# Kernel optimization log

Hardware: AMD Instinct MI355X
Metric: run time of the kernel (lower is better)

Reference implementation:

```python
import jax, jax.numpy as jnp
import numpy as np

N = 50000   # nodes
E = 640000  # edges
IN = 128
HID = 128
EPS = 1e-5


def setup_inputs() -> dict:
    key = jax.random.key(0)
    ks = jax.random.split(key, 8)
    s = 1.0 / np.sqrt(IN)
    inp = {
        "x": jax.random.normal(ks[0], (N, IN), jnp.float32),
        "src": jax.random.randint(ks[1], (E,), 0, N, dtype=jnp.int32),
        "dst": jax.random.randint(ks[2], (E,), 0, N, dtype=jnp.int32),
        "W1": jax.random.normal(ks[3], (IN, HID), jnp.float32) * s,
        "b1": jnp.zeros((HID,), jnp.float32),
        "g1": jnp.ones((HID,), jnp.float32),
        "be1": jnp.zeros((HID,), jnp.float32),
        "W2": jax.random.normal(ks[4], (HID, HID), jnp.float32) * s,
        "b2": jnp.zeros((HID,), jnp.float32),
        "g2": jnp.ones((HID,), jnp.float32),
        "be2": jnp.zeros((HID,), jnp.float32),
        "W3": jax.random.normal(ks[5], (HID, HID), jnp.float32) * s,
        "b3": jnp.zeros((HID,), jnp.float32),
        "g3": jnp.ones((HID,), jnp.float32),
        "be3": jnp.zeros((HID,), jnp.float32),
    }
    return inp


def _layernorm(h, g, b):
    mu = jnp.mean(h, axis=-1, keepdims=True)
    var = jnp.mean(jnp.square(h - mu), axis=-1, keepdims=True)
    return g * (h - mu) * jax.lax.rsqrt(var + EPS) + b


def _gcn_conv(h, W, b, src, dst):
    # Kipf & Welling GCN: D^{-1/2} (A + I) D^{-1/2} (H W) + b
    # self-loops added with weight 1; degree computed on the target index.
    hw = h @ W                                          # [N, HID]
    deg = jax.ops.segment_sum(jnp.ones((E,), h.dtype), dst, num_segments=N) + 1.0
    dinv = jax.lax.rsqrt(deg)                           # deg >= 1 due to self loop
    msg = hw[src] * (dinv[src] * dinv[dst])[:, None]    # gather + normalize, [E, HID]
    agg = jax.ops.segment_sum(msg, dst, num_segments=N)  # scatter-add
    agg = agg + hw * (dinv * dinv)[:, None]             # self-loop contribution
    return agg + b


def reference(x, src, dst, W1, b1, g1, be1, W2, b2, g2, be2, W3, b3, g3, be3):
    layers = [(W1, b1, g1, be1), (W2, b2, g2, be2), (W3, b3, g3, be3)]
    h = x
    for i, (W, b, g, be) in enumerate(layers):
        h_in = h
        h = _gcn_conv(h, W, b, src, dst)
        h = _layernorm(h, g, be)
        h = jax.nn.relu(h)
        # dropout: eval mode -> identity
        if i > 0 and h.shape == h_in.shape:
            h = h + h_in
    return h
```

## Files before the change

kernel.cpp:

```cpp
#include <hip/hip_runtime.h>
#include <hip/hip_bf16.h>

#define NFEAT 128
#define EPSLN 1e-5f
#define PAD 64

typedef __attribute__((ext_vector_type(8))) short short8;
typedef __attribute__((ext_vector_type(4))) float f32x4;

__device__ __forceinline__ float bf2f(ushort u) {
    union { uint u32; float f; } v; v.u32 = ((uint)u) << 16; return v.f;
}
__device__ __forceinline__ ushort f2bf(float f) {
    union { float f; uint u32; } v; v.f = f;
    uint u = v.u32;
    u += 0x7FFF + ((u >> 16) & 1);
    return (ushort)(u >> 16);
}

__global__ void setup_kernel(const float* __restrict__ x, ushort* __restrict__ xb, int n4,
                             int4* __restrict__ cnt4, int ncnt4,
                             const float* __restrict__ W0, const float* __restrict__ W1,
                             const float* __restrict__ W2,
                             ushort* __restrict__ Wt0, ushort* __restrict__ Wt1,
                             ushort* __restrict__ Wt2) {
    int i = blockIdx.x * 256 + threadIdx.x;
    if (i < n4) {
        float4 v = ((const float4*)x)[i];
        ushort4 o;
        o.x = f2bf(v.x); o.y = f2bf(v.y); o.z = f2bf(v.z); o.w = f2bf(v.w);
        ((ushort4*)xb)[i] = o;
    }
    if (i < ncnt4) cnt4[i] = make_int4(0, 0, 0, 0);
    if (i < 3 * NFEAT * NFEAT) {
        int l = i / (NFEAT * NFEAT);
        int r = i - l * (NFEAT * NFEAT);
        int k = r >> 7, n = r & 127;
        const float* W = (l == 0) ? W0 : (l == 1) ? W1 : W2;
        ushort* Wt = (l == 0) ? Wt0 : (l == 1) ? Wt1 : Wt2;
        Wt[n * NFEAT + k] = f2bf(W[r]);
    }
}

__global__ void fill_kernel(const int* __restrict__ src, const int* __restrict__ dst,
                            int* __restrict__ cnt, int* __restrict__ csr, int E) {
    int e = blockIdx.x * 256 + threadIdx.x;
    if (e < E) {
        int d = dst[e];
        int s = src[e];
        int pos = atomicAdd(&cnt[d], 1);
        if (pos < PAD) csr[d * PAD + pos] = s;
    }
}

__global__ __launch_bounds__(256) void gemm_mfma_kernel(const ushort* __restrict__ hb,
                                                        const ushort* __restrict__ Wt,
                                                        const int* __restrict__ cnt,
                                                        ushort* __restrict__ hw, int N) {
    __shared__ ushort WtL[NFEAT * NFEAT];
    {
        const uint4* src4 = (const uint4*)Wt;
        uint4* dst4 = (uint4*)WtL;
        #pragma unroll
        for (int i = 0; i < 8; ++i)
            dst4[threadIdx.x + i * 256] = src4[threadIdx.x + i * 256];
    }
    __syncthreads();

    const int wave = threadIdx.x >> 6;
    const int lane = threadIdx.x & 63;
    const int quad = lane >> 4;
    const int l16  = lane & 15;
    const int row0 = blockIdx.x * 128 + wave * 32;

    short8 afrag[2][4];
    #pragma unroll
    for (int t = 0; t < 2; ++t) {
        const int arow = row0 + t * 16 + l16;
        const short8* ap = (const short8*)(hb + (size_t)arow * NFEAT);
        const bool rowok = (arow < N);
        #pragma unroll
        for (int ks = 0; ks < 4; ++ks) {
            if (rowok) afrag[t][ks] = ap[ks * 4 + quad];
            else       afrag[t][ks] = short8{0, 0, 0, 0, 0, 0, 0, 0};
        }
    }

    f32x4 acc[2][8];
    #pragma unroll
    for (int t = 0; t < 2; ++t)
        #pragma unroll
        for (int ct = 0; ct < 8; ++ct) acc[t][ct] = f32x4{0.f, 0.f, 0.f, 0.f};

    #pragma unroll
    for (int ct = 0; ct < 8; ++ct) {
        const int bcol = ct * 16 + l16;
        const short8* bp = (const short8*)(WtL + (size_t)bcol * NFEAT);
        #pragma unroll
        for (int ks = 0; ks < 4; ++ks) {
            short8 bfrag = bp[ks * 4 + quad];
            acc[0][ct] = __builtin_amdgcn_mfma_f32_16x16x32_bf16(afrag[0][ks], bfrag, acc[0][ct], 0, 0, 0);
            acc[1][ct] = __builtin_amdgcn_mfma_f32_16x16x32_bf16(afrag[1][ks], bfrag, acc[1][ct], 0, 0, 0);
        }
    }

    #pragma unroll
    for (int t = 0; t < 2; ++t) {
        const int orow_base = row0 + t * 16 + quad * 4;
        #pragma unroll
        for (int r = 0; r < 4; ++r) {
            const int orow = orow_base + r;
            if (orow < N) {
                const float di = rsqrtf((float)cnt[orow] + 1.0f);
                ushort* op = hw + (size_t)orow * NFEAT + l16;
                #pragma unroll
                for (int ct = 0; ct < 8; ++ct)
                    op[ct * 16] = f2bf(acc[t][ct][r] * di);
            }
        }
    }
}

__global__ __launch_bounds__(256) void agg_ln_kernel(const ushort* __restrict__ hwb,
                                                     const int* __restrict__ cnt,
                                                     const int* __restrict__ csr,
                                                     const float* __restrict__ bias,
                                                     const float* __restrict__ gamma,
                                                     const float* __restrict__ beta,
                                                     const ushort* __restrict__ hres_b,
                                                     float* __restrict__ outf,
                                                     ushort* __restrict__ outb,
                                                     int N) {
    const int node = blockIdx.x * 4 + (threadIdx.x >> 6);
    const int lane = threadIdx.x & 63;
    if (node >= N) return;
    const int quad = lane >> 4;
    const int l16  = lane & 15;

    const int cn  = cnt[node];
    const int deg = (cn < PAD) ? cn : PAD;
    const float di = rsqrtf((float)cn + 1.0f);
    const int* ce = csr + (size_t)node * PAD;
    const uint4* hw4 = (const uint4*)hwb;

    float acc[8];
    #pragma unroll
    for (int i = 0; i < 8; ++i) acc[i] = 0.f;

    const int ng = (deg + 7) >> 3;
    for (int gi = 0; gi < ng; ++gi) {
        const int j0 = gi * 8 + quad;
        const int j1 = j0 + 4;
        int s0 = 0, s1 = 0;
        float w0 = 0.f, w1 = 0.f;
        if (j0 < deg) { s0 = ce[j0]; w0 = 1.f; }
        if (j1 < deg) { s1 = ce[j1]; w1 = 1.f; }
        uint4 v0 = hw4[(size_t)s0 * 16 + l16];
        uint4 v1 = hw4[(size_t)s1 * 16 + l16];
        acc[0] = fmaf(bf2f((ushort)(v0.x & 0xFFFF)), w0, acc[0]);
        acc[1] = fmaf(bf2f((ushort)(v0.x >> 16)),   w0, acc[1]);
        acc[2] = fmaf(bf2f((ushort)(v0.y & 0xFFFF)), w0, acc[2]);
        acc[3] = fmaf(bf2f((ushort)(v0.y >> 16)),   w0, acc[3]);
        acc[4] = fmaf(bf2f((ushort)(v0.z & 0xFFFF)), w0, acc[4]);
        acc[5] = fmaf(bf2f((ushort)(v0.z >> 16)),   w0, acc[5]);
        acc[6] = fmaf(bf2f((ushort)(v0.w & 0xFFFF)), w0, acc[6]);
        acc[7] = fmaf(bf2f((ushort)(v0.w >> 16)),   w0, acc[7]);
        acc[0] = fmaf(bf2f((ushort)(v1.x & 0xFFFF)), w1, acc[0]);
        acc[1] = fmaf(bf2f((ushort)(v1.x >> 16)),   w1, acc[1]);
        acc[2] = fmaf(bf2f((ushort)(v1.y & 0xFFFF)), w1, acc[2]);
        acc[3] = fmaf(bf2f((ushort)(v1.y >> 16)),   w1, acc[3]);
        acc[4] = fmaf(bf2f((ushort)(v1.z & 0xFFFF)), w1, acc[4]);
        acc[5] = fmaf(bf2f((ushort)(v1.z >> 16)),   w1, acc[5]);
        acc[6] = fmaf(bf2f((ushort)(v1.w & 0xFFFF)), w1, acc[6]);
        acc[7] = fmaf(bf2f((ushort)(v1.w >> 16)),   w1, acc[7]);
    }

    #pragma unroll
    for (int i = 0; i < 8; ++i) {
        acc[i] += __shfl_xor(acc[i], 16);
        acc[i] += __shfl_xor(acc[i], 32);
    }

    const int c0i = l16 * 8;
    uint4 hv = hw4[(size_t)node * 16 + l16];
    float4 b0 = ((const float4*)(bias + c0i))[0];
    float4 b1 = ((const float4*)(bias + c0i))[1];
    float x[8];
    x[0] = (acc[0] + bf2f((ushort)(hv.x & 0xFFFF))) * di + b0.x;
    x[1] = (acc[1] + bf2f((ushort)(hv.x >> 16)))   * di + b0.y;
    x[2] = (acc[2] + bf2f((ushort)(hv.y & 0xFFFF))) * di + b0.z;
    x[3] = (acc[3] + bf2f((ushort)(hv.y >> 16)))   * di + b0.w;
    x[4] = (acc[4] + bf2f((ushort)(hv.z & 0xFFFF))) * di + b1.x;
    x[5] = (acc[5] + bf2f((ushort)(hv.z >> 16)))   * di + b1.y;
    x[6] = (acc[6] + bf2f((ushort)(hv.w & 0xFFFF))) * di + b1.z;
    x[7] = (acc[7] + bf2f((ushort)(hv.w >> 16)))   * di + b1.w;

    float s = 0.f, sq = 0.f;
    #pragma unroll
    for (int i = 0; i < 8; ++i) { s += x[i]; sq += x[i] * x[i]; }
    #pragma unroll
    for (int o = 8; o > 0; o >>= 1) {
        s  += __shfl_xor(s, o);
        sq += __shfl_xor(sq, o);
    }
    const float mu  = s * (1.0f / NFEAT);
    const float var = sq * (1.0f / NFEAT) - mu * mu;
    const float rs  = rsqrtf(var + EPSLN);

    float4 g0 = ((const float4*)(gamma + c0i))[0];
    float4 g1 = ((const float4*)(gamma + c0i))[1];
    float4 e0 = ((const float4*)(beta + c0i))[0];
    float4 e1 = ((const float4*)(beta + c0i))[1];
    float gm[8] = {g0.x, g0.y, g0.z, g0.w, g1.x, g1.y, g1.z, g1.w};
    float bt[8] = {e0.x, e0.y, e0.z, e0.w, e1.x, e1.y, e1.z, e1.w};

    float y[8];
    #pragma unroll
    for (int i = 0; i < 8; ++i)
        y[i] = fmaxf(gm[i] * (x[i] - mu) * rs + bt[i], 0.0f);

    if (hres_b) {
        uint4 hr = ((const uint4*)hres_b)[(size_t)node * 16 + l16];
        y[0] += bf2f((ushort)(hr.x & 0xFFFF));
        y[1] += bf2f((ushort)(hr.x >> 16));
        y[2] += bf2f((ushort)(hr.y & 0xFFFF));
        y[3] += bf2f((ushort)(hr.y >> 16));
        y[4] += bf2f((ushort)(hr.z & 0xFFFF));
        y[5] += bf2f((ushort)(hr.z >> 16));
        y[6] += bf2f((ushort)(hr.w & 0xFFFF));
        y[7] += bf2f((ushort)(hr.w >> 16));
    }

    if (quad == 0) {
        if (outf) {
            float4* op = (float4*)(outf + (size_t)node * NFEAT + c0i);
            op[0] = make_float4(y[0], y[1], y[2], y[3]);
            op[1] = make_float4(y[4], y[5], y[6], y[7]);
        }
        if (outb) {
            uint4 ob;
            ob.x = (uint)f2bf(y[0]) | ((uint)f2bf(y[1]) << 16);
            ob.y = (uint)f2bf(y[2]) | ((uint)f2bf(y[3]) << 16);
            ob.z = (uint)f2bf(y[4]) | ((uint)f2bf(y[5]) << 16);
            ob.w = (uint)f2bf(y[6]) | ((uint)f2bf(y[7]) << 16);
            ((uint4*)outb)[(size_t)node * 16 + l16] = ob;
        }
    }
}

extern "C" void kernel_launch(void* const* d_in, const int* in_sizes, int n_in,
                              void* d_out, int out_size, void* d_ws, size_t ws_size,
                              hipStream_t stream) {
    const float* x   = (const float*)d_in[0];
    const int*   src = (const int*)d_in[1];
    const int*   dst = (const int*)d_in[2];
    const float* W[3]  = {(const float*)d_in[3], (const float*)d_in[7],  (const float*)d_in[11]};
    const float* b[3]  = {(const float*)d_in[4], (const float*)d_in[8],  (const float*)d_in[12]};
    const float* g[3]  = {(const float*)d_in[5], (const float*)d_in[9],  (const float*)d_in[13]};
    const float* be[3] = {(const float*)d_in[6], (const float*)d_in[10], (const float*)d_in[14]};

    const int N = in_sizes[0] / NFEAT;
    const int E = in_sizes[1];

    char* ws = (char*)d_ws;
    size_t off = 0;
    auto carve = [&](size_t bytes) -> char* {
        char* p = ws + off;
        off = (off + bytes + 255) & ~(size_t)255;
        return p;
    };
    const int ncnt4 = (N + 3) / 4;
    int*    cnt = (int*)   carve((size_t)ncnt4 * 4 * sizeof(int));
    int*    csr = (int*)   carve(((size_t)N * PAD + 64) * sizeof(int));
    ushort* hwb = (ushort*)carve((size_t)N * NFEAT * sizeof(ushort));
    ushort* xb  = (ushort*)carve((size_t)N * NFEAT * sizeof(ushort));
    ushort* h1b = (ushort*)carve((size_t)N * NFEAT * sizeof(ushort));
    ushort* h2b = (ushort*)carve((size_t)N * NFEAT * sizeof(ushort));
    ushort* Wt[3];
    for (int l = 0; l < 3; ++l) Wt[l] = (ushort*)carve(NFEAT * NFEAT * sizeof(ushort));
    (void)ws_size;

    const int n4 = N * NFEAT / 4;
    int setup_threads = n4;
    if (3 * NFEAT * NFEAT > setup_threads) setup_threads = 3 * NFEAT * NFEAT;
    if (ncnt4 > setup_threads) setup_threads = ncnt4;
    setup_kernel<<<(setup_threads + 255) / 256, 256, 0, stream>>>(
        x, xb, n4, (int4*)cnt, ncnt4, W[0], W[1], W[2], Wt[0], Wt[1], Wt[2]);

    fill_kernel<<<(E + 255) / 256, 256, 0, stream>>>(src, dst, cnt, csr, E);

    const ushort* hbin[3]  = {xb, h1b, h2b};
    const ushort* hresb[3] = {nullptr, h1b, h2b};
    float*        houtf[3] = {nullptr, nullptr, (float*)d_out};
    ushort*       houtb[3] = {h1b, h2b, nullptr};

    const int gemm_blocks = (N + 127) / 128;
    const int agg_blocks = (N + 3) / 4;

    for (int l = 0; l < 3; ++l) {
        gemm_mfma_kernel<<<gemm_blocks, 256, 0, stream>>>(hbin[l], Wt[l], cnt, hwb, N);
        agg_ln_kernel<<<agg_blocks, 256, 0, stream>>>(hwb, cnt, csr,
                                                      b[l], g[l], be[l],
                                                      hresb[l], houtf[l], houtb[l], N);
    }
}
```

Before: 282.7 us.

## Fuse x bf16 conversion into first GEMM, shrink GEMM tile, deepen gather unroll

The standalone fp32-to-bf16 conversion of x is removed from the setup kernel. The first-layer GEMM now reads fp32 x directly and converts it in registers, which drops a full write and re-read of the intermediate bf16 buffer. The GEMM tile shrinks from 128 to 64 rows per block (16 rows per wave), giving twice as many blocks but less reuse of the LDS-resident weights. The aggregation kernel issues four neighbor gathers per iteration instead of two and hoists the self, bias, gamma, beta and residual loads ahead of the gather loop to add memory-level parallelism, at the cost of more registers.

```diff
diff --git a/kernel.cpp b/kernel.cpp
--- a/kernel.cpp
+++ b/kernel.cpp
@@ -18,19 +18,12 @@
     return (ushort)(u >> 16);
 }
 
-__global__ void setup_kernel(const float* __restrict__ x, ushort* __restrict__ xb, int n4,
-                             int4* __restrict__ cnt4, int ncnt4,
+__global__ void setup_kernel(int4* __restrict__ cnt4, int ncnt4,
                              const float* __restrict__ W0, const float* __restrict__ W1,
                              const float* __restrict__ W2,
                              ushort* __restrict__ Wt0, ushort* __restrict__ Wt1,
                              ushort* __restrict__ Wt2) {
     int i = blockIdx.x * 256 + threadIdx.x;
-    if (i < n4) {
-        float4 v = ((const float4*)x)[i];
-        ushort4 o;
-        o.x = f2bf(v.x); o.y = f2bf(v.y); o.z = f2bf(v.z); o.w = f2bf(v.w);
-        ((ushort4*)xb)[i] = o;
-    }
     if (i < ncnt4) cnt4[i] = make_int4(0, 0, 0, 0);
     if (i < 3 * NFEAT * NFEAT) {
         int l = i / (NFEAT * NFEAT);
@@ -54,6 +47,7 @@
 }
 
 __global__ __launch_bounds__(256) void gemm_mfma_kernel(const ushort* __restrict__ hb,
+                                                        const float* __restrict__ hf,
                                                         const ushort* __restrict__ Wt,
                                                         const int* __restrict__ cnt,
                                                         ushort* __restrict__ hw, int N) {
@@ -71,26 +65,38 @@
     const int lane = threadIdx.x & 63;
     const int quad = lane >> 4;
     const int l16  = lane & 15;
-    const int row0 = blockIdx.x * 128 + wave * 32;
-
-    short8 afrag[2][4];
-    #pragma unroll
-    for (int t = 0; t < 2; ++t) {
-        const int arow = row0 + t * 16 + l16;
+    const int row0 = blockIdx.x * 64 + wave * 16;
+    const int arow = row0 + l16;
+    const bool rowok = (arow < N);
+
+    short8 afrag[4];
+    if (hf) {
+        const float4* fp = (const float4*)(hf + (size_t)arow * NFEAT);
+        #pragma unroll
+        for (int ks = 0; ks < 4; ++ks) {
+            short8 a = short8{0, 0, 0, 0, 0, 0, 0, 0};
+            if (rowok) {
+                float4 u0 = fp[ks * 8 + quad * 2];
+                float4 u1 = fp[ks * 8 + quad * 2 + 1];
+                a[0] = (short)f2bf(u0.x); a[1] = (short)f2bf(u0.y);
+                a[2] = (short)f2bf(u0.z); a[3] = (short)f2bf(u0.w);
+                a[4] = (short)f2bf(u1.x); a[5] = (short)f2bf(u1.y);
+                a[6] = (short)f2bf(u1.z); a[7] = (short)f2bf(u1.w);
+            }
+            afrag[ks] = a;
+        }
+    } else {
         const short8* ap = (const short8*)(hb + (size_t)arow * NFEAT);
-        const bool rowok = (arow < N);
         #pragma unroll
         for (int ks = 0; ks < 4; ++ks) {
-            if (rowok) afrag[t][ks] = ap[ks * 4 + quad];
-            else       afrag[t][ks] = short8{0, 0, 0, 0, 0, 0, 0, 0};
-        }
-    }
-
-    f32x4 acc[2][8];
-    #pragma unroll
-    for (int t = 0; t < 2; ++t)
-        #pragma unroll
-        for (int ct = 0; ct < 8; ++ct) acc[t][ct] = f32x4{0.f, 0.f, 0.f, 0.f};
+            if (rowok) afrag[ks] = ap[ks * 4 + quad];
+            else       afrag[ks] = short8{0, 0, 0, 0, 0, 0, 0, 0};
+        }
+    }
+
+    f32x4 acc[8];
+    #pragma unroll
+    for (int ct = 0; ct < 8; ++ct) acc[ct] = f32x4{0.f, 0.f, 0.f, 0.f};
 
     #pragma unroll
     for (int ct = 0; ct < 8; ++ct) {
@@ -99,24 +105,20 @@
         #pragma unroll
         for (int ks = 0; ks < 4; ++ks) {
             short8 bfrag = bp[ks * 4 + quad];
-            acc[0][ct] = __builtin_amdgcn_mfma_f32_16x16x32_bf16(afrag[0][ks], bfrag, acc[0][ct], 0, 0, 0);
-            acc[1][ct] = __builtin_amdgcn_mfma_f32_16x16x32_bf16(afrag[1][ks], bfrag, acc[1][ct], 0, 0, 0);
-        }
-    }
-
-    #pragma unroll
-    for (int t = 0; t < 2; ++t) {
-        const int orow_base = row0 + t * 16 + quad * 4;
-        #pragma unroll
-        for (int r = 0; r < 4; ++r) {
-            const int orow = orow_base + r;
-            if (orow < N) {
-                const float di = rsqrtf((float)cnt[orow] + 1.0f);
-                ushort* op = hw + (size_t)orow * NFEAT + l16;
-                #pragma unroll
-                for (int ct = 0; ct < 8; ++ct)
-                    op[ct * 16] = f2bf(acc[t][ct][r] * di);
-            }
+            acc[ct] = __builtin_amdgcn_mfma_f32_16x16x32_bf16(afrag[ks], bfrag, acc[ct], 0, 0, 0);
+        }
+    }
+
+    const int orow_base = row0 + quad * 4;
+    #pragma unroll
+    for (int r = 0; r < 4; ++r) {
+        const int orow = orow_base + r;
+        if (orow < N) {
+            const float di = rsqrtf((float)cnt[orow] + 1.0f);
+            ushort* op = hw + (size_t)orow * NFEAT + l16;
+            #pragma unroll
+            for (int ct = 0; ct < 8; ++ct)
+                op[ct * 16] = f2bf(acc[ct][r] * di);
         }
     }
 }
@@ -136,6 +138,7 @@
     if (node >= N) return;
     const int quad = lane >> 4;
     const int l16  = lane & 15;
+    const int c0i  = l16 * 8;
 
     const int cn  = cnt[node];
     const int deg = (cn < PAD) ? cn : PAD;
@@ -143,36 +146,67 @@
     const int* ce = csr + (size_t)node * PAD;
     const uint4* hw4 = (const uint4*)hwb;
 
+    uint4 hv = hw4[(size_t)node * 16 + l16];
+    float4 b0 = ((const float4*)(bias + c0i))[0];
+    float4 b1 = ((const float4*)(bias + c0i))[1];
+    float4 g0 = ((const float4*)(gamma + c0i))[0];
+    float4 g1 = ((const float4*)(gamma + c0i))[1];
+    float4 e0 = ((const float4*)(beta + c0i))[0];
+    float4 e1 = ((const float4*)(beta + c0i))[1];
+    uint4 hr = make_uint4(0, 0, 0, 0);
+    if (hres_b) hr = ((const uint4*)hres_b)[(size_t)node * 16 + l16];
+
     float acc[8];
     #pragma unroll
     for (int i = 0; i < 8; ++i) acc[i] = 0.f;
 
-    const int ng = (deg + 7) >> 3;
+    const int ng = (deg + 15) >> 4;
     for (int gi = 0; gi < ng; ++gi) {
-        const int j0 = gi * 8 + quad;
-        const int j1 = j0 + 4;
-        int s0 = 0, s1 = 0;
-        float w0 = 0.f, w1 = 0.f;
-        if (j0 < deg) { s0 = ce[j0]; w0 = 1.f; }
-        if (j1 < deg) { s1 = ce[j1]; w1 = 1.f; }
-        uint4 v0 = hw4[(size_t)s0 * 16 + l16];
-        uint4 v1 = hw4[(size_t)s1 * 16 + l16];
-        acc[0] = fmaf(bf2f((ushort)(v0.x & 0xFFFF)), w0, acc[0]);
-        acc[1] = fmaf(bf2f((ushort)(v0.x >> 16)),   w0, acc[1]);
-        acc[2] = fmaf(bf2f((ushort)(v0.y & 0xFFFF)), w0, acc[2]);
-        acc[3] = fmaf(bf2f((ushort)(v0.y >> 16)),   w0, acc[3]);
-        acc[4] = fmaf(bf2f((ushort)(v0.z & 0xFFFF)), w0, acc[4]);
-        acc[5] = fmaf(bf2f((ushort)(v0.z >> 16)),   w0, acc[5]);
-        acc[6] = fmaf(bf2f((ushort)(v0.w & 0xFFFF)), w0, acc[6]);
-        acc[7] = fmaf(bf2f((ushort)(v0.w >> 16)),   w0, acc[7]);
-        acc[0] = fmaf(bf2f((ushort)(v1.x & 0xFFFF)), w1, acc[0]);
-        acc[1] = fmaf(bf2f((ushort)(v1.x >> 16)),   w1, acc[1]);
-        acc[2] = fmaf(bf2f((ushort)(v1.y & 0xFFFF)), w1, acc[2]);
-        acc[3] = fmaf(bf2f((ushort)(v1.y >> 16)),   w1, acc[3]);
-        acc[4] = fmaf(bf2f((ushort)(v1.z & 0xFFFF)), w1, acc[4]);
-        acc[5] = fmaf(bf2f((ushort)(v1.z >> 16)),   w1, acc[5]);
-        acc[6] = fmaf(bf2f((ushort)(v1.w & 0xFFFF)), w1, acc[6]);
-        acc[7] = fmaf(bf2f((ushort)(v1.w >> 16)),   w1, acc[7]);
+        const int jb = gi * 16 + quad;
+        int   s[4];
+        float w[4];
+        #pragma unroll
+        for (int u = 0; u < 4; ++u) {
+            const int j = jb + u * 4;
+            if (j < deg) { s[u] = ce[j]; w[u] = 1.f; }
+            else         { s[u] = 0;     w[u] = 0.f; }
+        }
+        uint4 v0 = hw4[(size_t)s[0] * 16 + l16];
+        uint4 v1 = hw4[(size_t)s[1] * 16 + l16];
+        uint4 v2 = hw4[(size_t)s[2] * 16 + l16];
+        uint4 v3 = hw4[(size_t)s[3] * 16 + l16];
+        acc[0] = fmaf(bf2f((ushort)(v0.x & 0xFFFF)), w[0], acc[0]);
+        acc[1] = fmaf(bf2f((ushort)(v0.x >> 16)),   w[0], acc[1]);
+        acc[2] = fmaf(bf2f((ushort)(v0.y & 0xFFFF)), w[0], acc[2]);
+        acc[3] = fmaf(bf2f((ushort)(v0.y >> 16)),   w[0], acc[3]);
+        acc[4] = fmaf(bf2f((ushort)(v0.z & 0xFFFF)), w[0], acc[4]);
+        acc[5] = fmaf(bf2f((ushort)(v0.z >> 16)),   w[0], acc[5]);
+        acc[6] = fmaf(bf2f((ushort)(v0.w & 0xFFFF)), w[0], acc[6]);
+        acc[7] = fmaf(bf2f((ushort)(v0.w >> 16)),   w[0], acc[7]);
+        acc[0] = fmaf(bf2f((ushort)(v1.x & 0xFFFF)), w[1], acc[0]);
+        acc[1] = fmaf(bf2f((ushort)(v1.x >> 16)),   w[1], acc[1]);
+        acc[2] = fmaf(bf2f((ushort)(v1.y & 0xFFFF)), w[1], acc[2]);
+        acc[3] = fmaf(bf2f((ushort)(v1.y >> 16)),   w[1], acc[3]);
+        acc[4] = fmaf(bf2f((ushort)(v1.z & 0xFFFF)), w[1], acc[4]);
+        acc[5] = fmaf(bf2f((ushort)(v1.z >> 16)),   w[1], acc[5]);
+        acc[6] = fmaf(bf2f((ushort)(v1.w & 0xFFFF)), w[1], acc[6]);
+        acc[7] = fmaf(bf2f((ushort)(v1.w >> 16)),   w[1], acc[7]);
+        acc[0] = fmaf(bf2f((ushort)(v2.x & 0xFFFF)), w[2], acc[0]);
+        acc[1] = fmaf(bf2f((ushort)(v2.x >> 16)),   w[2], acc[1]);
+        acc[2] = fmaf(bf2f((ushort)(v2.y & 0xFFFF)), w[2], acc[2]);
+        acc[3] = fmaf(bf2f((ushort)(v2.y >> 16)),   w[2], acc[3]);
+        acc[4] = fmaf(bf2f((ushort)(v2.z & 0xFFFF)), w[2], acc[4]);
+        acc[5] = fmaf(bf2f((ushort)(v2.z >> 16)),   w[2], acc[5]);
+        acc[6] = fmaf(bf2f((ushort)(v2.w & 0xFFFF)), w[2], acc[6]);
+        acc[7] = fmaf(bf2f((ushort)(v2.w >> 16)),   w[2], acc[7]);
+        acc[0] = fmaf(bf2f((ushort)(v3.x & 0xFFFF)), w[3], acc[0]);
+        acc[1] = fmaf(bf2f((ushort)(v3.x >> 16)),   w[3], acc[1]);
+        acc[2] = fmaf(bf2f((ushort)(v3.y & 0xFFFF)), w[3], acc[2]);
+        acc[3] = fmaf(bf2f((ushort)(v3.y >> 16)),   w[3], acc[3]);
+        acc[4] = fmaf(bf2f((ushort)(v3.z & 0xFFFF)), w[3], acc[4]);
+        acc[5] = fmaf(bf2f((ushort)(v3.z >> 16)),   w[3], acc[5]);
+        acc[6] = fmaf(bf2f((ushort)(v3.w & 0xFFFF)), w[3], acc[6]);
+        acc[7] = fmaf(bf2f((ushort)(v3.w >> 16)),   w[3], acc[7]);
     }
 
     #pragma unroll
@@ -181,10 +215,6 @@
         acc[i] += __shfl_xor(acc[i], 32);
     }
 
-    const int c0i = l16 * 8;
-    uint4 hv = hw4[(size_t)node * 16 + l16];
-    float4 b0 = ((const float4*)(bias + c0i))[0];
-    float4 b1 = ((const float4*)(bias + c0i))[1];
     float x[8];
     x[0] = (acc[0] + bf2f((ushort)(hv.x & 0xFFFF))) * di + b0.x;
     x[1] = (acc[1] + bf2f((ushort)(hv.x >> 16)))   * di + b0.y;
@@ -207,10 +237,6 @@
     const float var = sq * (1.0f / NFEAT) - mu * mu;
     const float rs  = rsqrtf(var + EPSLN);
 
-    float4 g0 = ((const float4*)(gamma + c0i))[0];
-    float4 g1 = ((const float4*)(gamma + c0i))[1];
-    float4 e0 = ((const float4*)(beta + c0i))[0];
-    float4 e1 = ((const float4*)(beta + c0i))[1];
     float gm[8] = {g0.x, g0.y, g0.z, g0.w, g1.x, g1.y, g1.z, g1.w};
     float bt[8] = {e0.x, e0.y, e0.z, e0.w, e1.x, e1.y, e1.z, e1.w};
 
@@ -220,7 +246,6 @@
         y[i] = fmaxf(gm[i] * (x[i] - mu) * rs + bt[i], 0.0f);
 
     if (hres_b) {
-        uint4 hr = ((const uint4*)hres_b)[(size_t)node * 16 + l16];
         y[0] += bf2f((ushort)(hr.x & 0xFFFF));
         y[1] += bf2f((ushort)(hr.x >> 16));
         y[2] += bf2f((ushort)(hr.y & 0xFFFF));
@@ -273,32 +298,30 @@
     int*    cnt = (int*)   carve((size_t)ncnt4 * 4 * sizeof(int));
     int*    csr = (int*)   carve(((size_t)N * PAD + 64) * sizeof(int));
     ushort* hwb = (ushort*)carve((size_t)N * NFEAT * sizeof(ushort));
-    ushort* xb  = (ushort*)carve((size_t)N * NFEAT * sizeof(ushort));
     ushort* h1b = (ushort*)carve((size_t)N * NFEAT * sizeof(ushort));
     ushort* h2b = (ushort*)carve((size_t)N * NFEAT * sizeof(ushort));
     ushort* Wt[3];
     for (int l = 0; l < 3; ++l) Wt[l] = (ushort*)carve(NFEAT * NFEAT * sizeof(ushort));
     (void)ws_size;
 
-    const int n4 = N * NFEAT / 4;
-    int setup_threads = n4;
-    if (3 * NFEAT * NFEAT > setup_threads) setup_threads = 3 * NFEAT * NFEAT;
+    int setup_threads = 3 * NFEAT * NFEAT;
     if (ncnt4 > setup_threads) setup_threads = ncnt4;
     setup_kernel<<<(setup_threads + 255) / 256, 256, 0, stream>>>(
-        x, xb, n4, (int4*)cnt, ncnt4, W[0], W[1], W[2], Wt[0], Wt[1], Wt[2]);
+        (int4*)cnt, ncnt4, W[0], W[1], W[2], Wt[0], Wt[1], Wt[2]);
 
     fill_kernel<<<(E + 255) / 256, 256, 0, stream>>>(src, dst, cnt, csr, E);
 
-    const ushort* hbin[3]  = {xb, h1b, h2b};
+    const ushort* hbin[3]  = {nullptr, h1b, h2b};
+    const float*  hfin[3]  = {x, nullptr, nullptr};
     const ushort* hresb[3] = {nullptr, h1b, h2b};
     float*        houtf[3] = {nullptr, nullptr, (float*)d_out};
     ushort*       houtb[3] = {h1b, h2b, nullptr};
 
-    const int gemm_blocks = (N + 127) / 128;
+    const int gemm_blocks = (N + 63) / 64;
     const int agg_blocks = (N + 3) / 4;
 
     for (int l = 0; l < 3; ++l) {
-        gemm_mfma_kernel<<<gemm_blocks, 256, 0, stream>>>(hbin[l], Wt[l], cnt, hwb, N);
+        gemm_mfma_kernel<<<gemm_blocks, 256, 0, stream>>>(hbin[l], hfin[l], Wt[l], cnt, hwb, N);
         agg_ln_kernel<<<agg_blocks, 256, 0, stream>>>(hwb, cnt, csr,
                                                       b[l], g[l], be[l],
                                                       hresb[l], houtf[l], houtb[l], N);
```

After: 307.7 us. 8.9% more time.
